# Performance work log

Hardware: AMD Instinct MI355X
Metric: run time of the kernel (lower is better)

Reference implementation:

```python
import jax, jax.numpy as jnp
import numpy as np

N_NODES = 50000
N_EDGES = 800000
IN_DIM, HID, OUT = 512, 96, 64


def gcn_conv(x, W, b, src, dst, n_nodes):
    # PyG GCNConv: h = x W; aggregate with sym-normalized adjacency incl. self-loops; add bias.
    h = x @ W  # [N, out]
    ones = jnp.ones_like(dst, dtype=h.dtype)
    deg = jax.ops.segment_sum(ones, dst, num_segments=n_nodes) + 1.0  # +1 for self-loop
    dinv = jax.lax.rsqrt(deg)
    norm = dinv[src] * dinv[dst]  # [E]
    agg = jax.ops.segment_sum(h[src] * norm[:, None], dst, num_segments=n_nodes)
    agg = agg + h * (dinv * dinv)[:, None]  # self-loop messages
    return agg + b


def setup_inputs() -> dict:
    key = jax.random.key(0)
    ks = jax.random.split(key, 12)
    s = 0.05
    x = jax.random.normal(ks[0], (N_NODES, IN_DIM), jnp.float32)
    edge_index = jax.random.randint(ks[1], (2, N_EDGES), 0, N_NODES)
    return {
        "x": x,
        "edge_index": edge_index,
        "W0": jax.random.normal(ks[2], (IN_DIM, HID), jnp.float32) * s,
        "b0": jnp.zeros((HID,), jnp.float32),
        "W1": jax.random.normal(ks[3], (HID, HID), jnp.float32) * s,
        "b1": jnp.zeros((HID,), jnp.float32),
        "W2": jax.random.normal(ks[4], (HID, HID), jnp.float32) * s,
        "b2": jnp.zeros((HID,), jnp.float32),
        "fcW": jax.random.normal(ks[5], (HID, OUT), jnp.float32) * s,
        "fcb": jnp.zeros((OUT,), jnp.float32),
    }


def reference(x, edge_index, W0, b0, W1, b1, W2, b2, fcW, fcb):
    src, dst = edge_index[0], edge_index[1]
    n = x.shape[0]
    # eval mode: dropout is identity; bn=False so no batchnorm
    h = jax.nn.relu(gcn_conv(x, W0, b0, src, dst, n))
    h = jax.nn.relu(gcn_conv(h, W1, b1, src, dst, n))
    h = jax.nn.relu(gcn_conv(h, W2, b2, src, dst, n))
    out = h @ fcW + fcb
    return jnp.squeeze(out)
```

## Files before the change

### kernel.cpp

```cpp
#include <hip/hip_runtime.h>


constexpr int NN   = 50000;
constexpr int NE   = 800000;
constexpr int KIN  = 512;
constexpr int HIDD = 96;
constexpr int ODIM = 64;
constexpr int NBLK = (NN + 255) / 256;
constexpr int GB   = (NN + 63) / 64;
constexpr int SB   = (NE + 511) / 512;
constexpr int HB   = (NE + 255) / 256;

typedef short bf16x8 __attribute__((ext_vector_type(8)));
typedef short s8v    __attribute__((ext_vector_type(8)));
typedef float f32x4  __attribute__((ext_vector_type(4)));
typedef _Float16 h8  __attribute__((ext_vector_type(8)));

__device__ inline short f2bf(float f) {
    union { float f; unsigned u; } v; v.f = f;
    unsigned r = v.u + 0x7FFFu + ((v.u >> 16) & 1u);
    return (short)(r >> 16);
}
__device__ inline short f2bf_trunc(float f) {
    union { float f; unsigned u; } v; v.f = f;
    return (short)(v.u >> 16);
}
__device__ inline float bf2f(short h) {
    union { unsigned u; float f; } v; v.u = ((unsigned)(unsigned short)h) << 16;
    return v.f;
}

__global__ void hist_pack(const int* __restrict__ dst, int* __restrict__ deg,
                          int* __restrict__ rank,
                          const float* __restrict__ W0, const float* __restrict__ W1,
                          const float* __restrict__ W2, const float* __restrict__ FC,
                          short* __restrict__ w0hi, short* __restrict__ w0lo,
                          short* __restrict__ w1hi, short* __restrict__ w1lo,
                          short* __restrict__ w2hi, short* __restrict__ w2lo,
                          short* __restrict__ fchi, short* __restrict__ fclo) {
    if (blockIdx.x < HB) {
        const int e = blockIdx.x * 256 + threadIdx.x;
        if (e < NE) rank[e] = atomicAdd(&deg[dst[e]], 1);
        return;
    }
    const int idx = (blockIdx.x - HB) * 256 + threadIdx.x;
    const float* W; short *hi, *lo; int M, li;
    if      (idx < 49152) { W = W0; hi = w0hi; lo = w0lo; M = 96; li = idx; }
    else if (idx < 58368) { W = W1; hi = w1hi; lo = w1lo; M = 96; li = idx - 49152; }
    else if (idx < 67584) { W = W2; hi = w2hi; lo = w2lo; M = 96; li = idx - 58368; }
    else if (idx < 73728) { W = FC; hi = fchi; lo = fclo; M = 64; li = idx - 67584; }
    else return;
    const int CT = M >> 4;
    const int j = li & 7;
    const int lane = (li >> 3) & 63;
    const int t = li >> 9;
    const int ct = t % CT;
    const int kc = t / CT;
    const int k = kc * 32 + (lane >> 4) * 8 + j;
    const int n = ct * 16 + (lane & 15);
    const float w = W[k * M + n];
    const short h = f2bf(w);
    hi[li] = h;
    lo[li] = f2bf_trunc(w - bf2f(h));
}

__global__ void scan1_kernel(const int* __restrict__ deg, int* __restrict__ excl,
                             int* __restrict__ partials) {
    __shared__ int tmp[256];
    const int tid = threadIdx.x;
    const int i = blockIdx.x * 256 + tid;
    const int v = (i < NN) ? deg[i] : 0;
    tmp[tid] = v;
    __syncthreads();
#pragma unroll
    for (int off = 1; off < 256; off <<= 1) {
        int t = (tid >= off) ? tmp[tid - off] : 0;
        __syncthreads();
        tmp[tid] += t;
        __syncthreads();
    }
    if (i < NN) excl[i] = tmp[tid] - v;
    if (tid == 255) partials[blockIdx.x] = tmp[tid];
}

__global__ void scan3_kernel(const int* __restrict__ excl, const int* __restrict__ partials,
                             const int* __restrict__ deg, int* __restrict__ rowstart,
                             float* __restrict__ dinv) {
    __shared__ int tmp[256];
    const int tid = threadIdx.x;
    tmp[tid] = (tid < (int)blockIdx.x) ? partials[tid] : 0;
    __syncthreads();
#pragma unroll
    for (int off = 128; off > 0; off >>= 1) {
        if (tid < off) tmp[tid] += tmp[tid + off];
        __syncthreads();
    }
    const int boff = tmp[0];
    const int i = blockIdx.x * 256 + tid;
    if (i < NN) {
        rowstart[i] = excl[i] + boff;
        dinv[i] = 1.0f / sqrtf((float)deg[i] + 1.0f);
    }
    if (blockIdx.x == 0 && tid == 0) rowstart[NN] = NE;
}

template <int K>
__launch_bounds__(512, 6)
__global__ void gemm_scatter(const float* __restrict__ A, const short* __restrict__ Whi,
                             const short* __restrict__ Wlo, const float* __restrict__ dinv,
                             _Float16* __restrict__ C, int N,
                             const int* __restrict__ src, const int* __restrict__ dst,
                             const int* __restrict__ rank, const int* __restrict__ rowstart,
                             int* __restrict__ csr_src) {
    constexpr int CT = 6;
    constexpr int KCH = K / 64;
    constexpr int PH  = KCH / 2;
    __shared__ short sHi[4 * 3072];
    __shared__ short sLo[4 * 3072];

    const int tid = threadIdx.x;

    if (blockIdx.x >= GB) {
        const int e = (blockIdx.x - GB) * 512 + tid;
        if (e < NE) {
            const int d = dst[e];
            csr_src[rowstart[d] + rank[e]] = src[e];
        }
        return;
    }

    const int lane = tid & 63;
    const int wave = tid >> 6;
    const int rw = wave & 3;
    const int kh = wave >> 2;
    const int q = lane >> 4;
    const int m = lane & 15;
    const int row = blockIdx.x * 64 + rw * 16 + m;
    const int arow = (row < N) ? row : (N - 1);

    f32x4 acc[CT];
#pragma unroll
    for (int c = 0; c < CT; ++c) acc[c] = f32x4{0.f, 0.f, 0.f, 0.f};

    const float* ap = A + (size_t)arow * K + kh * (K / 2) + q * 8;
    float4 a0 = *(const float4*)(ap);
    float4 a1 = *(const float4*)(ap + 4);

#pragma unroll
    for (int p = 0; p < PH; ++p) {
#pragma unroll
        for (int i = 0; i < 3; ++i) {
            const int ci = i * 512 + tid;
            const int slot = ci / 384;
            const int within = ci - slot * 384;
            const int kcg = (slot >> 1) * KCH + p * 2 + (slot & 1);
            const int so = kcg * 3072 + within * 8;
            const int doff = ci * 8;
            *(float4*)(sHi + doff) = *(const float4*)(Whi + so);
            *(float4*)(sLo + doff) = *(const float4*)(Wlo + so);
        }
        __syncthreads();

#pragma unroll
        for (int kc = 0; kc < 2; ++kc) {
            const float af[8] = {a0.x, a0.y, a0.z, a0.w, a1.x, a1.y, a1.z, a1.w};
            bf16x8 ahi, alo;
#pragma unroll
            for (int j = 0; j < 8; ++j) {
                const short h = f2bf(af[j]);
                ahi[j] = h;
                alo[j] = f2bf_trunc(af[j] - bf2f(h));
            }
            if (p * 2 + kc + 1 < KCH) {
                ap += 32;
                a0 = *(const float4*)(ap);
                a1 = *(const float4*)(ap + 4);
            }
            const int slot = kh * 2 + kc;
            const short* hbase = sHi + slot * 3072 + lane * 8;
            const short* lbase = sLo + slot * 3072 + lane * 8;
#pragma unroll
            for (int c = 0; c < CT; ++c) {
                const bf16x8 wh = *(const bf16x8*)(hbase + c * 512);
                const bf16x8 wl = *(const bf16x8*)(lbase + c * 512);
                acc[c] = __builtin_amdgcn_mfma_f32_16x16x32_bf16(ahi, wh, acc[c], 0, 0, 0);
                acc[c] = __builtin_amdgcn_mfma_f32_16x16x32_bf16(alo, wh, acc[c], 0, 0, 0);
                acc[c] = __builtin_amdgcn_mfma_f32_16x16x32_bf16(ahi, wl, acc[c], 0, 0, 0);
            }
        }
        __syncthreads();
    }

    float* sAcc = (float*)sHi;
    if (kh == 1) {
#pragma unroll
        for (int c = 0; c < CT; ++c)
            *(f32x4*)(sAcc + ((rw * 64 + lane) * CT + c) * 4) = acc[c];
    }
    __syncthreads();
    if (kh == 0) {
#pragma unroll
        for (int c = 0; c < CT; ++c) {
            const f32x4 o = *(const f32x4*)(sAcc + ((rw * 64 + lane) * CT + c) * 4);
            acc[c][0] += o[0]; acc[c][1] += o[1]; acc[c][2] += o[2]; acc[c][3] += o[3];
        }
        const int rbase = blockIdx.x * 64 + rw * 16 + q * 4;
#pragma unroll
        for (int r = 0; r < 4; ++r) {
            const int orow = rbase + r;
            if (orow < N) {
                const float s = dinv[orow];
#pragma unroll
                for (int c = 0; c < CT; ++c)
                    C[(size_t)orow * 96 + c * 16 + m] = (_Float16)(acc[c][r] * s);
            }
        }
    }
}

constexpr int APAD = 104;
template <int M, bool FC>
__launch_bounds__(768, 6)
__global__ void fused_gg(const int* __restrict__ rowstart, const float* __restrict__ dinv,
                         const int* __restrict__ csr_src, const _Float16* __restrict__ hs,
                         const float* __restrict__ gb,
                         const short* __restrict__ Whi, const short* __restrict__ Wlo,
                         const float* __restrict__ bias2,
                         _Float16* __restrict__ Ch, float* __restrict__ Cf, int N) {
    constexpr int CT = M / 16;
    __shared__ short sAhi[64 * APAD];
    __shared__ short sAlo[64 * APAD];

    const int tid = threadIdx.x;
    const int nb = blockIdx.x * 64;
    const int nl = tid / 12;
    const int fl = tid - nl * 12;
    const int node = nb + nl;

    s8v hi8, lo8;
    if (node < N) {
        const _Float16* __restrict__ hp = hs + fl * 8;
        float acc0[8], acc1[8];
        {
            const h8 sv = *(const h8*)(hp + (size_t)node * 96);
#pragma unroll
            for (int e = 0; e < 8; ++e) { acc0[e] = (float)sv[e]; acc1[e] = 0.f; }
        }
        int j = rowstart[node];
        const int jend = rowstart[node + 1];
        for (; j + 8 <= jend; j += 8) {
            const int s0 = csr_src[j],     s1 = csr_src[j + 1];
            const int s2 = csr_src[j + 2], s3 = csr_src[j + 3];
            const int s4 = csr_src[j + 4], s5 = csr_src[j + 5];
            const int s6 = csr_src[j + 6], s7 = csr_src[j + 7];
            const h8 v0 = *(const h8*)(hp + (size_t)s0 * 96);
            const h8 v1 = *(const h8*)(hp + (size_t)s1 * 96);
            const h8 v2 = *(const h8*)(hp + (size_t)s2 * 96);
            const h8 v3 = *(const h8*)(hp + (size_t)s3 * 96);
            const h8 v4 = *(const h8*)(hp + (size_t)s4 * 96);
            const h8 v5 = *(const h8*)(hp + (size_t)s5 * 96);
            const h8 v6 = *(const h8*)(hp + (size_t)s6 * 96);
            const h8 v7 = *(const h8*)(hp + (size_t)s7 * 96);
#pragma unroll
            for (int e = 0; e < 8; ++e) {
                acc0[e] += ((float)v0[e] + (float)v4[e]) + ((float)v2[e] + (float)v6[e]);
                acc1[e] += ((float)v1[e] + (float)v5[e]) + ((float)v3[e] + (float)v7[e]);
            }
        }
        if (j + 4 <= jend) {
            const int s0 = csr_src[j], s1 = csr_src[j + 1];
            const int s2 = csr_src[j + 2], s3 = csr_src[j + 3];
            const h8 v0 = *(const h8*)(hp + (size_t)s0 * 96);
            const h8 v1 = *(const h8*)(hp + (size_t)s1 * 96);
            const h8 v2 = *(const h8*)(hp + (size_t)s2 * 96);
            const h8 v3 = *(const h8*)(hp + (size_t)s3 * 96);
#pragma unroll
            for (int e = 0; e < 8; ++e) {
                acc0[e] += (float)v0[e] + (float)v2[e];
                acc1[e] += (float)v1[e] + (float)v3[e];
            }
            j += 4;
        }
        if (j + 2 <= jend) {
            const int s0 = csr_src[j], s1 = csr_src[j + 1];
            const h8 v0 = *(const h8*)(hp + (size_t)s0 * 96);
            const h8 v1 = *(const h8*)(hp + (size_t)s1 * 96);
#pragma unroll
            for (int e = 0; e < 8; ++e) {
                acc0[e] += (float)v0[e];
                acc1[e] += (float)v1[e];
            }
            j += 2;
        }
        if (j < jend) {
            const h8 v0 = *(const h8*)(hp + (size_t)csr_src[j] * 96);
#pragma unroll
            for (int e = 0; e < 8; ++e) acc0[e] += (float)v0[e];
        }
        const float di = dinv[node];
#pragma unroll
        for (int e = 0; e < 8; ++e) {
            const float o = fmaxf(fmaf(di, acc0[e] + acc1[e], gb[fl * 8 + e]), 0.0f);
            const short h = f2bf(o);
            hi8[e] = h;
            lo8[e] = f2bf_trunc(o - bf2f(h));
        }
    } else {
#pragma unroll
        for (int e = 0; e < 8; ++e) { hi8[e] = 0; lo8[e] = 0; }
    }
    *(s8v*)(sAhi + nl * APAD + fl * 8) = hi8;
    *(s8v*)(sAlo + nl * APAD + fl * 8) = lo8;
    __syncthreads();

    const int lane = tid & 63;
    const int wave = tid >> 6;
    const int rw = wave & 3;
    const int c0 = (wave >> 2) * 2;
    const int q = lane >> 4;
    const int m = lane & 15;

    if (c0 < CT) {
        bf16x8 Ah[3], Al[3];
#pragma unroll
        for (int kc = 0; kc < 3; ++kc) {
            const int off = (rw * 16 + m) * APAD + kc * 32 + q * 8;
            Ah[kc] = *(const bf16x8*)(sAhi + off);
            Al[kc] = *(const bf16x8*)(sAlo + off);
        }

        f32x4 gacc[2];
        gacc[0] = f32x4{0.f, 0.f, 0.f, 0.f};
        gacc[1] = f32x4{0.f, 0.f, 0.f, 0.f};

#pragma unroll
        for (int kc = 0; kc < 3; ++kc) {
#pragma unroll
            for (int c = 0; c < 2; ++c) {
                const int fo = ((kc * CT + c0 + c) * 64 + lane) * 8;
                const bf16x8 wh = *(const bf16x8*)(Whi + fo);
                const bf16x8 wl = *(const bf16x8*)(Wlo + fo);
                gacc[c] = __builtin_amdgcn_mfma_f32_16x16x32_bf16(Ah[kc], wh, gacc[c], 0, 0, 0);
                gacc[c] = __builtin_amdgcn_mfma_f32_16x16x32_bf16(Al[kc], wh, gacc[c], 0, 0, 0);
                gacc[c] = __builtin_amdgcn_mfma_f32_16x16x32_bf16(Ah[kc], wl, gacc[c], 0, 0, 0);
            }
        }

        const int rbase = nb + rw * 16 + q * 4;
#pragma unroll
        for (int r = 0; r < 4; ++r) {
            const int orow = rbase + r;
            if (orow < N) {
                if (FC) {
#pragma unroll
                    for (int c = 0; c < 2; ++c)
                        Cf[(size_t)orow * M + (c0 + c) * 16 + m] = gacc[c][r] + bias2[(c0 + c) * 16 + m];
                } else {
                    const float s = dinv[orow];
#pragma unroll
                    for (int c = 0; c < 2; ++c)
                        Ch[(size_t)orow * M + (c0 + c) * 16 + m] = (_Float16)(gacc[c][r] * s);
                }
            }
        }
    }
}

extern "C" void kernel_launch(void* const* d_in, const int* in_sizes, int n_in,
                              void* d_out, int out_size, void* d_ws, size_t ws_size,
                              hipStream_t stream) {
    const float* x   = (const float*)d_in[0];
    const int*   ei  = (const int*)d_in[1];
    const float* W0  = (const float*)d_in[2];
    const float* b0  = (const float*)d_in[3];
    const float* W1  = (const float*)d_in[4];
    const float* b1  = (const float*)d_in[5];
    const float* W2  = (const float*)d_in[6];
    const float* b2  = (const float*)d_in[7];
    const float* fcW = (const float*)d_in[8];
    const float* fcb = (const float*)d_in[9];
    float* out = (float*)d_out;

    const int* src = ei;
    const int* dst = ei + NE;

    float* ws = (float*)d_ws;
    float* dinv     = ws;
    int*   deg      = (int*)(ws + 50176);
    int*   excl     = (int*)(ws + 100352);
    int*   rowstart = (int*)(ws + 200704);
    int*   partials = (int*)(ws + 250880);
    int*   csr_src  = (int*)(ws + 251136);
    short* w0hi = (short*)(ws + 1051392);
    short* w0lo = (short*)(ws + 1075968);
    short* w1hi = (short*)(ws + 1100544);
    short* w1lo = (short*)(ws + 1105152);
    short* w2hi = (short*)(ws + 1109760);
    short* w2lo = (short*)(ws + 1114368);
    short* fchi = (short*)(ws + 1118976);
    short* fclo = (short*)(ws + 1122048);
    _Float16* hsA = (_Float16*)(ws + 1125120);
    _Float16* hsB = (_Float16*)(ws + 3525120);
    int*   rank    = (int*)(ws + 5925120);

    dim3 b256(256);
    const int gHP = HB + (73728 + 255) / 256;
    const int gGS = GB + SB;
    const int gFus = GB;

    hipMemsetAsync(deg, 0, NN * sizeof(int), stream);
    hist_pack<<<gHP, b256, 0, stream>>>(dst, deg, rank, W0, W1, W2, fcW,
                                        w0hi, w0lo, w1hi, w1lo,
                                        w2hi, w2lo, fchi, fclo);
    scan1_kernel<<<NBLK, b256, 0, stream>>>(deg, excl, partials);
    scan3_kernel<<<NBLK, b256, 0, stream>>>(excl, partials, deg, rowstart, dinv);

    gemm_scatter<KIN><<<gGS, dim3(512), 0, stream>>>(x, w0hi, w0lo, dinv, hsA, NN,
                                                     src, dst, rank, rowstart, csr_src);

    fused_gg<HIDD, false><<<gFus, dim3(768), 0, stream>>>(
        rowstart, dinv, csr_src, hsA, b0, w1hi, w1lo, nullptr, hsB, nullptr, NN);

    fused_gg<HIDD, false><<<gFus, dim3(768), 0, stream>>>(
        rowstart, dinv, csr_src, hsB, b1, w2hi, w2lo, nullptr, hsA, nullptr, NN);

    fused_gg<ODIM, true><<<gFus, dim3(768), 0, stream>>>(
        rowstart, dinv, csr_src, hsA, b2, fchi, fclo, fcb, nullptr, out, NN);
}
```

Baseline: 335.3 us.

## Drop LDS staging and K-split in first GEMM, read weights from global

```diff
diff --git a/kernel.cpp b/kernel.cpp
--- a/kernel.cpp
+++ b/kernel.cpp
@@ -8,7 +8,7 @@
 constexpr int ODIM = 64;
 constexpr int NBLK = (NN + 255) / 256;
 constexpr int GB   = (NN + 63) / 64;
-constexpr int SB   = (NE + 511) / 512;
+constexpr int SB   = (NE + 1023) / 1024;
 constexpr int HB   = (NE + 255) / 256;
 
 typedef short bf16x8 __attribute__((ext_vector_type(8)));
@@ -105,115 +105,76 @@
 }
 
 template <int K>
-__launch_bounds__(512, 6)
+__launch_bounds__(256, 4)
 __global__ void gemm_scatter(const float* __restrict__ A, const short* __restrict__ Whi,
                              const short* __restrict__ Wlo, const float* __restrict__ dinv,
                              _Float16* __restrict__ C, int N,
                              const int* __restrict__ src, const int* __restrict__ dst,
                              const int* __restrict__ rank, const int* __restrict__ rowstart,
                              int* __restrict__ csr_src) {
-    constexpr int CT = 6;
-    constexpr int KCH = K / 64;
-    constexpr int PH  = KCH / 2;
-    __shared__ short sHi[4 * 3072];
-    __shared__ short sLo[4 * 3072];
-
+    constexpr int CT  = 6;
+    constexpr int KCH = K / 32;
     const int tid = threadIdx.x;
 
     if (blockIdx.x >= GB) {
-        const int e = (blockIdx.x - GB) * 512 + tid;
-        if (e < NE) {
-            const int d = dst[e];
-            csr_src[rowstart[d] + rank[e]] = src[e];
+        const int base = (blockIdx.x - GB) * 1024 + tid;
+#pragma unroll
+        for (int u = 0; u < 4; ++u) {
+            const int e = base + u * 256;
+            if (e < NE) {
+                const int d = dst[e];
+                csr_src[rowstart[d] + rank[e]] = src[e];
+            }
         }
         return;
     }
 
     const int lane = tid & 63;
     const int wave = tid >> 6;
-    const int rw = wave & 3;
-    const int kh = wave >> 2;
     const int q = lane >> 4;
     const int m = lane & 15;
-    const int row = blockIdx.x * 64 + rw * 16 + m;
+    const int row = blockIdx.x * 64 + wave * 16 + m;
     const int arow = (row < N) ? row : (N - 1);
 
     f32x4 acc[CT];
 #pragma unroll
     for (int c = 0; c < CT; ++c) acc[c] = f32x4{0.f, 0.f, 0.f, 0.f};
 
-    const float* ap = A + (size_t)arow * K + kh * (K / 2) + q * 8;
-    float4 a0 = *(const float4*)(ap);
-    float4 a1 = *(const float4*)(ap + 4);
-
-#pragma unroll
-    for (int p = 0; p < PH; ++p) {
-#pragma unroll
-        for (int i = 0; i < 3; ++i) {
-            const int ci = i * 512 + tid;
-            const int slot = ci / 384;
-            const int within = ci - slot * 384;
-            const int kcg = (slot >> 1) * KCH + p * 2 + (slot & 1);
-            const int so = kcg * 3072 + within * 8;
-            const int doff = ci * 8;
-            *(float4*)(sHi + doff) = *(const float4*)(Whi + so);
-            *(float4*)(sLo + doff) = *(const float4*)(Wlo + so);
-        }
-        __syncthreads();
-
-#pragma unroll
-        for (int kc = 0; kc < 2; ++kc) {
-            const float af[8] = {a0.x, a0.y, a0.z, a0.w, a1.x, a1.y, a1.z, a1.w};
-            bf16x8 ahi, alo;
-#pragma unroll
-            for (int j = 0; j < 8; ++j) {
-                const short h = f2bf(af[j]);
-                ahi[j] = h;
-                alo[j] = f2bf_trunc(af[j] - bf2f(h));
-            }
-            if (p * 2 + kc + 1 < KCH) {
-                ap += 32;
-                a0 = *(const float4*)(ap);
-                a1 = *(const float4*)(ap + 4);
-            }
-            const int slot = kh * 2 + kc;
-            const short* hbase = sHi + slot * 3072 + lane * 8;
-            const short* lbase = sLo + slot * 3072 + lane * 8;
-#pragma unroll
-            for (int c = 0; c < CT; ++c) {
-                const bf16x8 wh = *(const bf16x8*)(hbase + c * 512);
-                const bf16x8 wl = *(const bf16x8*)(lbase + c * 512);
-                acc[c] = __builtin_amdgcn_mfma_f32_16x16x32_bf16(ahi, wh, acc[c], 0, 0, 0);
-                acc[c] = __builtin_amdgcn_mfma_f32_16x16x32_bf16(alo, wh, acc[c], 0, 0, 0);
-                acc[c] = __builtin_amdgcn_mfma_f32_16x16x32_bf16(ahi, wl, acc[c], 0, 0, 0);
-            }
-        }
-        __syncthreads();
-    }
-
-    float* sAcc = (float*)sHi;
-    if (kh == 1) {
-#pragma unroll
-        for (int c = 0; c < CT; ++c)
-            *(f32x4*)(sAcc + ((rw * 64 + lane) * CT + c) * 4) = acc[c];
-    }
-    __syncthreads();
-    if (kh == 0) {
+    const float* ap = A + (size_t)arow * K + q * 8;
+
+#pragma unroll 4
+    for (int kc = 0; kc < KCH; ++kc) {
+        const float4 a0 = *(const float4*)(ap + kc * 32);
+        const float4 a1 = *(const float4*)(ap + kc * 32 + 4);
+        const float af[8] = {a0.x, a0.y, a0.z, a0.w, a1.x, a1.y, a1.z, a1.w};
+        bf16x8 ahi, alo;
+#pragma unroll
+        for (int j = 0; j < 8; ++j) {
+            const short h = f2bf(af[j]);
+            ahi[j] = h;
+            alo[j] = f2bf_trunc(af[j] - bf2f(h));
+        }
+        const short* hb = Whi + (size_t)kc * CT * 512 + lane * 8;
+        const short* lb = Wlo + (size_t)kc * CT * 512 + lane * 8;
 #pragma unroll
         for (int c = 0; c < CT; ++c) {
-            const f32x4 o = *(const f32x4*)(sAcc + ((rw * 64 + lane) * CT + c) * 4);
-            acc[c][0] += o[0]; acc[c][1] += o[1]; acc[c][2] += o[2]; acc[c][3] += o[3];
-        }
-        const int rbase = blockIdx.x * 64 + rw * 16 + q * 4;
-#pragma unroll
-        for (int r = 0; r < 4; ++r) {
-            const int orow = rbase + r;
-            if (orow < N) {
-                const float s = dinv[orow];
-#pragma unroll
-                for (int c = 0; c < CT; ++c)
-                    C[(size_t)orow * 96 + c * 16 + m] = (_Float16)(acc[c][r] * s);
-            }
+            const bf16x8 wh = *(const bf16x8*)(hb + c * 512);
+            const bf16x8 wl = *(const bf16x8*)(lb + c * 512);
+            acc[c] = __builtin_amdgcn_mfma_f32_16x16x32_bf16(ahi, wh, acc[c], 0, 0, 0);
+            acc[c] = __builtin_amdgcn_mfma_f32_16x16x32_bf16(alo, wh, acc[c], 0, 0, 0);
+            acc[c] = __builtin_amdgcn_mfma_f32_16x16x32_bf16(ahi, wl, acc[c], 0, 0, 0);
+        }
+    }
+
+    const int rbase = blockIdx.x * 64 + wave * 16 + q * 4;
+#pragma unroll
+    for (int r = 0; r < 4; ++r) {
+        const int orow = rbase + r;
+        if (orow < N) {
+            const float s = dinv[orow];
+#pragma unroll
+            for (int c = 0; c < CT; ++c)
+                C[(size_t)orow * 96 + c * 16 + m] = (_Float16)(acc[c][r] * s);
         }
     }
 }
@@ -415,8 +376,8 @@
     scan1_kernel<<<NBLK, b256, 0, stream>>>(deg, excl, partials);
     scan3_kernel<<<NBLK, b256, 0, stream>>>(excl, partials, deg, rowstart, dinv);
 
-    gemm_scatter<KIN><<<gGS, dim3(512), 0, stream>>>(x, w0hi, w0lo, dinv, hsA, NN,
-                                                     src, dst, rank, rowstart, csr_src);
+    gemm_scatter<KIN><<<gGS, b256, 0, stream>>>(x, w0hi, w0lo, dinv, hsA, NN,
+                                                src, dst, rank, rowstart, csr_src);
 
     fused_gg<HIDD, false><<<gFus, dim3(768), 0, stream>>>(
         rowstart, dinv, csr_src, hsA, b0, w1hi, w1lo, nullptr, hsB, nullptr, NN);
```

After: 347.3 us. 1.04x slower.

## Bucket nodes by degree and process aggregation in degree-sorted order

Applied to the files above, without the earlier changes.

```diff
diff --git a/kernel.cpp b/kernel.cpp
--- a/kernel.cpp
+++ b/kernel.cpp
@@ -65,12 +65,14 @@
 }
 
 __global__ void scan1_kernel(const int* __restrict__ deg, int* __restrict__ excl,
-                             int* __restrict__ partials) {
+                             int* __restrict__ partials, int* __restrict__ gcnt) {
     __shared__ int tmp[256];
+    __shared__ int bcnt[64];
     const int tid = threadIdx.x;
     const int i = blockIdx.x * 256 + tid;
     const int v = (i < NN) ? deg[i] : 0;
     tmp[tid] = v;
+    if (tid < 64) bcnt[tid] = 0;
     __syncthreads();
 #pragma unroll
     for (int off = 1; off < 256; off <<= 1) {
@@ -81,14 +83,22 @@
     }
     if (i < NN) excl[i] = tmp[tid] - v;
     if (tid == 255) partials[blockIdx.x] = tmp[tid];
+    if (i < NN) atomicAdd(&bcnt[v < 63 ? v : 63], 1);
+    __syncthreads();
+    if (tid < 64 && bcnt[tid] > 0) atomicAdd(&gcnt[tid], bcnt[tid]);
 }
 
 __global__ void scan3_kernel(const int* __restrict__ excl, const int* __restrict__ partials,
                              const int* __restrict__ deg, int* __restrict__ rowstart,
-                             float* __restrict__ dinv) {
+                             float* __restrict__ dinv, const int* __restrict__ gcnt,
+                             int* __restrict__ gcur, int* __restrict__ perm) {
     __shared__ int tmp[256];
+    __shared__ int bstart[64];
+    __shared__ int lcnt[64];
+    __shared__ int lbase[64];
     const int tid = threadIdx.x;
     tmp[tid] = (tid < (int)blockIdx.x) ? partials[tid] : 0;
+    if (tid < 64) lcnt[tid] = 0;
     __syncthreads();
 #pragma unroll
     for (int off = 128; off > 0; off >>= 1) {
@@ -97,11 +107,33 @@
     }
     const int boff = tmp[0];
     const int i = blockIdx.x * 256 + tid;
+    int dg = 0;
     if (i < NN) {
+        dg = deg[i];
         rowstart[i] = excl[i] + boff;
-        dinv[i] = 1.0f / sqrtf((float)deg[i] + 1.0f);
+        dinv[i] = 1.0f / sqrtf((float)dg + 1.0f);
     }
     if (blockIdx.x == 0 && tid == 0) rowstart[NN] = NE;
+
+    if (tid < 64) {
+        const int bval = gcnt[tid];
+        int x = bval;
+#pragma unroll
+        for (int off = 1; off < 64; off <<= 1) {
+            const int y = __shfl_up(x, off);
+            if (tid >= off) x += y;
+        }
+        bstart[tid] = x - bval;
+    }
+    int b = 0, lrank = 0;
+    if (i < NN) {
+        b = dg < 63 ? dg : 63;
+        lrank = atomicAdd(&lcnt[b], 1);
+    }
+    __syncthreads();
+    if (tid < 64) lbase[tid] = (lcnt[tid] > 0) ? atomicAdd(&gcur[tid], lcnt[tid]) : 0;
+    __syncthreads();
+    if (i < NN) perm[bstart[b] + lbase[b] + lrank] = i;
 }
 
 template <int K>
@@ -225,7 +257,7 @@
                          const int* __restrict__ csr_src, const _Float16* __restrict__ hs,
                          const float* __restrict__ gb,
                          const short* __restrict__ Whi, const short* __restrict__ Wlo,
-                         const float* __restrict__ bias2,
+                         const float* __restrict__ bias2, const int* __restrict__ perm,
                          _Float16* __restrict__ Ch, float* __restrict__ Cf, int N) {
     constexpr int CT = M / 16;
     __shared__ short sAhi[64 * APAD];
@@ -235,10 +267,11 @@
     const int nb = blockIdx.x * 64;
     const int nl = tid / 12;
     const int fl = tid - nl * 12;
-    const int node = nb + nl;
+    const int nidx = nb + nl;
 
     s8v hi8, lo8;
-    if (node < N) {
+    if (nidx < N) {
+        const int node = perm[nidx];
         const _Float16* __restrict__ hp = hs + fl * 8;
         float acc0[8], acc1[8];
         {
@@ -349,8 +382,9 @@
         const int rbase = nb + rw * 16 + q * 4;
 #pragma unroll
         for (int r = 0; r < 4; ++r) {
-            const int orow = rbase + r;
-            if (orow < N) {
+            const int oidx = rbase + r;
+            if (oidx < N) {
+                const int orow = perm[oidx];
                 if (FC) {
 #pragma unroll
                     for (int c = 0; c < 2; ++c)
@@ -387,6 +421,8 @@
     float* ws = (float*)d_ws;
     float* dinv     = ws;
     int*   deg      = (int*)(ws + 50176);
+    int*   gcnt     = (int*)(ws + 100224);
+    int*   gcur     = (int*)(ws + 100288);
     int*   excl     = (int*)(ws + 100352);
     int*   rowstart = (int*)(ws + 200704);
     int*   partials = (int*)(ws + 250880);
@@ -402,28 +438,31 @@
     _Float16* hsA = (_Float16*)(ws + 1125120);
     _Float16* hsB = (_Float16*)(ws + 3525120);
     int*   rank    = (int*)(ws + 5925120);
+    int*   perm    = (int*)(ws + 6725120);
 
     dim3 b256(256);
     const int gHP = HB + (73728 + 255) / 256;
     const int gGS = GB + SB;
     const int gFus = GB;
 
-    hipMemsetAsync(deg, 0, NN * sizeof(int), stream);
+    hipMemsetAsync(deg, 0, (50176 + 128) * sizeof(int) - 50176 * 0, stream);
+    hipMemsetAsync(deg, 0, (100352 - 50176) * sizeof(float), stream);
     hist_pack<<<gHP, b256, 0, stream>>>(dst, deg, rank, W0, W1, W2, fcW,
                                         w0hi, w0lo, w1hi, w1lo,
                                         w2hi, w2lo, fchi, fclo);
-    scan1_kernel<<<NBLK, b256, 0, stream>>>(deg, excl, partials);
-    scan3_kernel<<<NBLK, b256, 0, stream>>>(excl, partials, deg, rowstart, dinv);
+    scan1_kernel<<<NBLK, b256, 0, stream>>>(deg, excl, partials, gcnt);
+    scan3_kernel<<<NBLK, b256, 0, stream>>>(excl, partials, deg, rowstart, dinv,
+                                            gcnt, gcur, perm);
 
     gemm_scatter<KIN><<<gGS, dim3(512), 0, stream>>>(x, w0hi, w0lo, dinv, hsA, NN,
                                                      src, dst, rank, rowstart, csr_src);
 
     fused_gg<HIDD, false><<<gFus, dim3(768), 0, stream>>>(
-        rowstart, dinv, csr_src, hsA, b0, w1hi, w1lo, nullptr, hsB, nullptr, NN);
+        rowstart, dinv, csr_src, hsA, b0, w1hi, w1lo, nullptr, perm, hsB, nullptr, NN);
 
     fused_gg<HIDD, false><<<gFus, dim3(768), 0, stream>>>(
-        rowstart, dinv, csr_src, hsB, b1, w2hi, w2lo, nullptr, hsA, nullptr, NN);
+        rowstart, dinv, csr_src, hsB, b1, w2hi, w2lo, nullptr, perm, hsA, nullptr, NN);
 
     fused_gg<ODIM, true><<<gFus, dim3(768), 0, stream>>>(
-        rowstart, dinv, csr_src, hsA, b2, fchi, fclo, fcb, nullptr, out, NN);
-}
+        rowstart, dinv, csr_src, hsA, b2, fchi, fclo, fcb, perm, nullptr, out, NN);
+}
```

Result: slower. 349.7 us (+4.3%).
